# Kernel tuning notes

Hardware: AMD Instinct MI355X
Metric: run time of the kernel (lower is better)

Reference implementation:

```python
import jax, jax.numpy as jnp
import numpy as np

C_IN = 64
C_MID = 4

def setup_inputs() -> dict:
    key = jax.random.key(0)
    k1, k2, k3, k4, k5 = jax.random.split(key, 5)
    trans_b = jax.random.normal(k1, (32, 64, 256, 256), dtype=jnp.float32)
    # SE squeeze/excite weights (effective 1x1 convs): down 64->4, up 4->64
    w_down = jax.random.normal(k2, (C_MID, C_IN), dtype=jnp.float32) * (1.0 / np.sqrt(C_IN))
    b_down = jax.random.normal(k3, (C_MID,), dtype=jnp.float32) * 0.01
    w_up = jax.random.normal(k4, (C_IN, C_MID), dtype=jnp.float32) * (1.0 / np.sqrt(C_MID))
    b_up = jax.random.normal(k5, (C_IN,), dtype=jnp.float32) * 0.01
    return {"trans_b": trans_b, "w_down": w_down, "b_down": b_down, "w_up": w_up, "b_up": b_up}

def reference(trans_b, w_down, b_down, w_up, b_up):
    # Squeeze: global average pool over spatial dims -> [B, C]
    pooled = jnp.mean(trans_b, axis=(2, 3))
    # Excite: channel MLP 64 -> 4 -> 64
    hidden = jax.nn.relu(jnp.einsum('bc,mc->bm', pooled, w_down) + b_down)  # [B, 4]
    scale = jax.nn.sigmoid(jnp.einsum('bm,cm->bc', hidden, w_up) + b_up)   # [B, 64]
    # Channel-wise rescale of input feature map
    return trans_b * scale[:, :, None, None]
```

## Files before the change

### kernel.cpp

```cpp
#include <hip/hip_runtime.h>
#include <math.h>

#define NB 32
#define NC 64
#define HW 65536
#define CMID 4
#define NPLANES (NB * NC)

__global__ __launch_bounds__(256) void se_pool(const float* __restrict__ in,
                                               float* __restrict__ pooled) {
    const int plane = blockIdx.x;
    const float4* p = (const float4*)(in + (size_t)plane * HW);

    float sum = 0.f;
    #pragma unroll 4
    for (int i = threadIdx.x; i < HW / 4; i += 256) {
        float4 v = p[i];
        sum += (v.x + v.y) + (v.z + v.w);
    }

    #pragma unroll
    for (int off = 32; off > 0; off >>= 1)
        sum += __shfl_down(sum, off, 64);

    __shared__ float ws[4];
    const int lane = threadIdx.x & 63;
    const int wid  = threadIdx.x >> 6;
    if (lane == 0) ws[wid] = sum;
    __syncthreads();
    if (threadIdx.x == 0) {
        float s = (ws[0] + ws[1]) + (ws[2] + ws[3]);
        pooled[plane] = s * (1.0f / (float)HW);
    }
}

__global__ __launch_bounds__(64) void se_mlp(const float* __restrict__ pooled,
                                             const float* __restrict__ w_down,
                                             const float* __restrict__ b_down,
                                             const float* __restrict__ w_up,
                                             const float* __restrict__ b_up,
                                             float* __restrict__ scale) {
    const int b = blockIdx.x;
    const int t = threadIdx.x;

    __shared__ float pb[NC];
    __shared__ float hid[CMID];

    pb[t] = pooled[b * NC + t];
    __syncthreads();

    if (t < CMID) {
        float s = b_down[t];
        #pragma unroll
        for (int c = 0; c < NC; ++c) s += pb[c] * w_down[t * NC + c];
        hid[t] = fmaxf(s, 0.f);
    }
    __syncthreads();

    float s = b_up[t];
    #pragma unroll
    for (int m = 0; m < CMID; ++m) s += hid[m] * w_up[t * CMID + m];
    scale[b * NC + t] = 1.0f / (1.0f + __expf(-s));
}

__global__ __launch_bounds__(256) void se_rescale(const float* __restrict__ in,
                                                  const float* __restrict__ scale,
                                                  float* __restrict__ out) {
    const size_t i = (size_t)blockIdx.x * 256 + threadIdx.x;
    const float s = scale[i >> 14];
    float4 v = ((const float4*)in)[i];
    v.x *= s; v.y *= s; v.z *= s; v.w *= s;
    ((float4*)out)[i] = v;
}

extern "C" void kernel_launch(void* const* d_in, const int* in_sizes, int n_in,
                              void* d_out, int out_size, void* d_ws, size_t ws_size,
                              hipStream_t stream) {
    const float* trans_b = (const float*)d_in[0];
    const float* w_down  = (const float*)d_in[1];
    const float* b_down  = (const float*)d_in[2];
    const float* w_up    = (const float*)d_in[3];
    const float* b_up    = (const float*)d_in[4];
    float* out = (float*)d_out;

    float* pooled = (float*)d_ws;
    float* scale  = pooled + NPLANES;

    se_pool<<<NPLANES, 256, 0, stream>>>(trans_b, pooled);
    se_mlp<<<NB, 64, 0, stream>>>(pooled, w_down, b_down, w_up, b_up, scale);

    const int n4 = NB * NC * HW / 4;
    se_rescale<<<n4 / 256, 256, 0, stream>>>(trans_b, scale, out);
}
```

Before: 926.6 us.

## Chunk batches so rescale rereads input from cache, fuse MLP into rescale

Processes the batch in chunks of 8 images, running pool then scale per chunk so the second read of each chunk's input can hit in the large last-level cache rather than DRAM. The channel MLP is recomputed per block inside the rescale kernel, removing a separate launch and the scale buffer. Planes are split into quarter blocks with partial sums, and outputs use nontemporal stores to avoid evicting the input. The cost is more launches and redundant MLP work per block.

```diff
diff --git a/kernel.cpp b/kernel.cpp
--- a/kernel.cpp
+++ b/kernel.cpp
@@ -5,17 +5,24 @@
 #define NC 64
 #define HW 65536
 #define CMID 4
-#define NPLANES (NB * NC)
+#define CHUNK_B 8
+#define CHUNK_PLANES (CHUNK_B * NC)
+#define NCHUNK (NB / CHUNK_B)
+#define QSIZE (HW / 4)
 
-__global__ __launch_bounds__(256) void se_pool(const float* __restrict__ in,
-                                               float* __restrict__ pooled) {
-    const int plane = blockIdx.x;
-    const float4* p = (const float4*)(in + (size_t)plane * HW);
+typedef float f4 __attribute__((ext_vector_type(4)));
+
+__global__ __launch_bounds__(256) void se_pool_chunk(const float* __restrict__ in,
+                                                     float* __restrict__ partial,
+                                                     int base_plane) {
+    const int plane = base_plane + (int)(blockIdx.x >> 2);
+    const int q     = blockIdx.x & 3;
+    const f4* p = (const f4*)(in + (size_t)plane * HW + (size_t)q * QSIZE);
 
     float sum = 0.f;
-    #pragma unroll 4
-    for (int i = threadIdx.x; i < HW / 4; i += 256) {
-        float4 v = p[i];
+    #pragma unroll
+    for (int i = 0; i < 16; ++i) {
+        f4 v = p[i * 256 + threadIdx.x];
         sum += (v.x + v.y) + (v.z + v.w);
     }
 
@@ -28,49 +35,59 @@
     const int wid  = threadIdx.x >> 6;
     if (lane == 0) ws[wid] = sum;
     __syncthreads();
-    if (threadIdx.x == 0) {
-        float s = (ws[0] + ws[1]) + (ws[2] + ws[3]);
-        pooled[plane] = s * (1.0f / (float)HW);
-    }
+    if (threadIdx.x == 0)
+        partial[plane * 4 + q] = (ws[0] + ws[1]) + (ws[2] + ws[3]);
 }
 
-__global__ __launch_bounds__(64) void se_mlp(const float* __restrict__ pooled,
-                                             const float* __restrict__ w_down,
-                                             const float* __restrict__ b_down,
-                                             const float* __restrict__ w_up,
-                                             const float* __restrict__ b_up,
-                                             float* __restrict__ scale) {
-    const int b = blockIdx.x;
-    const int t = threadIdx.x;
+__global__ __launch_bounds__(256) void se_scale_chunk(const float* __restrict__ in,
+                                                      const float* __restrict__ partial,
+                                                      const float* __restrict__ w_down,
+                                                      const float* __restrict__ b_down,
+                                                      const float* __restrict__ w_up,
+                                                      const float* __restrict__ b_up,
+                                                      float* __restrict__ out,
+                                                      int base_plane) {
+    const int plane = base_plane + (int)(blockIdx.x >> 2);
+    const int q     = blockIdx.x & 3;
+    const int b     = plane >> 6;
+    const int c     = plane & 63;
+    const int t     = threadIdx.x;
 
     __shared__ float pb[NC];
     __shared__ float hid[CMID];
+    __shared__ float s_scale;
 
-    pb[t] = pooled[b * NC + t];
+    if (t < NC) {
+        f4 pq = ((const f4*)partial)[b * NC + t];
+        pb[t] = (pq.x + pq.y + pq.z + pq.w) * (1.0f / (float)HW);
+    }
     __syncthreads();
 
     if (t < CMID) {
         float s = b_down[t];
         #pragma unroll
-        for (int c = 0; c < NC; ++c) s += pb[c] * w_down[t * NC + c];
+        for (int cc = 0; cc < NC; ++cc) s += pb[cc] * w_down[t * NC + cc];
         hid[t] = fmaxf(s, 0.f);
     }
     __syncthreads();
 
-    float s = b_up[t];
+    if (t == 0) {
+        float s = b_up[c];
+        #pragma unroll
+        for (int m = 0; m < CMID; ++m) s += hid[m] * w_up[c * CMID + m];
+        s_scale = 1.0f / (1.0f + __expf(-s));
+    }
+    __syncthreads();
+
+    const float s = s_scale;
+    const f4* ip = (const f4*)(in  + (size_t)plane * HW + (size_t)q * QSIZE);
+    f4*       op = (f4*)      (out + (size_t)plane * HW + (size_t)q * QSIZE);
     #pragma unroll
-    for (int m = 0; m < CMID; ++m) s += hid[m] * w_up[t * CMID + m];
-    scale[b * NC + t] = 1.0f / (1.0f + __expf(-s));
-}
-
-__global__ __launch_bounds__(256) void se_rescale(const float* __restrict__ in,
-                                                  const float* __restrict__ scale,
-                                                  float* __restrict__ out) {
-    const size_t i = (size_t)blockIdx.x * 256 + threadIdx.x;
-    const float s = scale[i >> 14];
-    float4 v = ((const float4*)in)[i];
-    v.x *= s; v.y *= s; v.z *= s; v.w *= s;
-    ((float4*)out)[i] = v;
+    for (int i = 0; i < 16; ++i) {
+        f4 v = ip[i * 256 + t];
+        v *= s;
+        __builtin_nontemporal_store(v, op + i * 256 + t);
+    }
 }
 
 extern "C" void kernel_launch(void* const* d_in, const int* in_sizes, int n_in,
@@ -83,12 +100,13 @@
     const float* b_up    = (const float*)d_in[4];
     float* out = (float*)d_out;
 
-    float* pooled = (float*)d_ws;
-    float* scale  = pooled + NPLANES;
+    float* partial = (float*)d_ws;
 
-    se_pool<<<NPLANES, 256, 0, stream>>>(trans_b, pooled);
-    se_mlp<<<NB, 64, 0, stream>>>(pooled, w_down, b_down, w_up, b_up, scale);
-
-    const int n4 = NB * NC * HW / 4;
-    se_rescale<<<n4 / 256, 256, 0, stream>>>(trans_b, scale, out);
+    for (int k = 0; k < NCHUNK; ++k) {
+        const int base = k * CHUNK_PLANES;
+        se_pool_chunk<<<CHUNK_PLANES * 4, 256, 0, stream>>>(trans_b, partial, base);
+        se_scale_chunk<<<CHUNK_PLANES * 4, 256, 0, stream>>>(trans_b, partial,
+                                                             w_down, b_down, w_up, b_up,
+                                                             out, base);
+    }
 }
```

Result: no change. 916.1 us (-1.1%).
